# Kernel tuning notes

Hardware: AMD Instinct MI355X
Metric: run time of the kernel (lower is better)

## Reference

```python
import jax, jax.numpy as jnp
import numpy as np

H, KVH, DH = 32, 8, 128        # attention heads, kv heads, head dim (shared by both streams)
G = H // KVH                   # GQA group size
EPS = 1e-6


def rms_norm(x, w):
    xf = x.astype(jnp.float32)
    n = xf * jax.lax.rsqrt(jnp.mean(xf * xf, axis=-1, keepdims=True) + EPS)
    return (n * w).astype(x.dtype)


def apply_rope(x, positions, max_wavelength=10000.0):
    # x: [B, L, h, DH], positions: [B, L]
    d_half = x.shape[-1] // 2
    freq_exponents = (2.0 / x.shape[-1]) * jnp.arange(d_half, dtype=jnp.float32)
    timescale = max_wavelength ** freq_exponents
    radians = positions[..., None].astype(jnp.float32) / timescale          # [B, L, d_half]
    radians = radians[..., None, :]                                         # [B, L, 1, d_half]
    s, c = jnp.sin(radians), jnp.cos(radians)
    xf = x.astype(jnp.float32)
    x1, x2 = xf[..., :d_half], xf[..., d_half:]
    out = jnp.concatenate([x1 * c - x2 * s, x2 * c + x1 * s], axis=-1)
    return out.astype(x.dtype)


def setup_inputs() -> dict:
    key = jax.random.key(0)
    ks = jax.random.split(key, 16)
    B, LV, LE = 2, 1024, 64
    DV, DE = 2560, 1920
    s = 0.02
    inp = {
        "vlm_embeds": jax.random.normal(ks[0], (B, LV, DV), jnp.float32),
        "expert_embeds": jax.random.normal(ks[1], (B, LE, DE), jnp.float32),
        "position_ids": jnp.sort(jax.random.randint(ks[2], (B, LV + LE), 0, 2048), axis=-1),
        "attention_mask": jnp.ones((B, LV + LE, LV + LE), dtype=bool),
        "w_ln_vlm": jnp.ones((DV,), jnp.float32),
        "Wq_vlm": jax.random.normal(ks[3], (DV, H * DH), jnp.float32) * s,
        "Wk_vlm": jax.random.normal(ks[4], (DV, KVH * DH), jnp.float32) * s,
        "Wv_vlm": jax.random.normal(ks[5], (DV, KVH * DH), jnp.float32) * s,
        "Wo_vlm": jax.random.normal(ks[6], (H * DH, DV), jnp.float32) * s,
        "w_ln_exp": jnp.ones((DE,), jnp.float32),
        "Wq_exp": jax.random.normal(ks[7], (DE, H * DH), jnp.float32) * s,
        "Wk_exp": jax.random.normal(ks[8], (DE, KVH * DH), jnp.float32) * s,
        "Wv_exp": jax.random.normal(ks[9], (DE, KVH * DH), jnp.float32) * s,
        "Wo_exp": jax.random.normal(ks[10], (H * DH, DE), jnp.float32) * s,
    }
    return inp


def _mixed_attn_layer(vlm_embeds, expert_embeds,
                      w_ln_vlm, Wq_vlm, Wk_vlm, Wv_vlm, Wo_vlm,
                      w_ln_exp, Wq_exp, Wk_exp, Wv_exp, Wo_exp,
                      position_ids, attention_mask, knowledge_insulation=True):
    B, LV, _ = vlm_embeds.shape
    LE = expert_embeds.shape[1]

    # Stream 0: VLM prefix (knowledge insulation -> no grad into VLM path).
    hv = rms_norm(vlm_embeds, w_ln_vlm)
    qv = (hv @ Wq_vlm).reshape(B, LV, H, DH)
    kv = (hv @ Wk_vlm).reshape(B, LV, KVH, DH)
    vv = (hv @ Wv_vlm).reshape(B, LV, KVH, DH)
    if knowledge_insulation:
        qv = jax.lax.stop_gradient(qv)
        kv = jax.lax.stop_gradient(kv)
        vv = jax.lax.stop_gradient(vv)

    # Stream 1: expert suffix.
    he = rms_norm(expert_embeds, w_ln_exp)
    qe = (he @ Wq_exp).reshape(B, LE, H, DH)
    ke = (he @ Wk_exp).reshape(B, LE, KVH, DH)
    ve = (he @ Wv_exp).reshape(B, LE, KVH, DH)

    # Concatenate streams along the sequence dim, then inline RoPE on q and k.
    q = jnp.concatenate([qv, qe], axis=1)          # [B, L, 32, 128]
    k = jnp.concatenate([kv, ke], axis=1)          # [B, L, 8, 128]
    v = jnp.concatenate([vv, ve], axis=1)
    q = apply_rope(q, position_ids)
    k = apply_rope(k, position_ids)

    # Eager GQA attention in fp32 (matches _eager_attention_forward).
    k_full = jnp.repeat(k, G, axis=2)              # kv-head major, group minor
    v_full = jnp.repeat(v, G, axis=2)
    att = jnp.einsum("bqhd,bkhd->bhqk", q.astype(jnp.float32), k_full.astype(jnp.float32))
    att = att * (DH ** -0.5)
    big_neg = jnp.finfo(jnp.float32).min
    att = jnp.where(attention_mask[:, None, :, :], att, big_neg)
    probs = jax.nn.softmax(att, axis=-1).astype(v_full.dtype)
    out = jnp.einsum("bhqk,bkhd->bqhd", probs, v_full).reshape(B, LV + LE, H * DH)

    # Split back to streams, per-stream output projection + residual.
    out_vlm = vlm_embeds + out[:, :LV] @ Wo_vlm
    out_exp = expert_embeds + out[:, LV:] @ Wo_exp
    return out_vlm, out_exp


def reference(vlm_embeds, expert_embeds, position_ids, attention_mask,
              w_ln_vlm, Wq_vlm, Wk_vlm, Wv_vlm, Wo_vlm,
              w_ln_exp, Wq_exp, Wk_exp, Wv_exp, Wo_exp):
    _, out_exp = _mixed_attn_layer(
        vlm_embeds, expert_embeds,
        w_ln_vlm, Wq_vlm, Wk_vlm, Wv_vlm, Wo_vlm,
        w_ln_exp, Wq_exp, Wk_exp, Wv_exp, Wo_exp,
        position_ids, attention_mask)
    return out_exp
```

## Files before the change

### kernel.cpp

```cpp
#include <hip/hip_runtime.h>
#include <hip/hip_bf16.h>
#include <cstddef>

#define B_  2
#define LV_ 1024
#define LE_ 64
#define S_TOT 1088
#define DV_ 2560
#define DE_ 1920
#define H_  32
#define KVH_ 8
#define DH_ 128
#define HD_ 4096
#define KVD_ 1024
#define NSPL 9

typedef short short8 __attribute__((ext_vector_type(8)));
typedef float f32x4 __attribute__((ext_vector_type(4)));

typedef __hip_bfloat16 bf16;

__device__ inline float b2f(bf16 h) { return __bfloat162float(h); }
__device__ inline bf16 f2b(float f) { return __float2bfloat16(f); }

#define OFF_HVB   0ul
#define OFF_WKVT  10485760ul
#define OFF_HEB   20971520ul
#define OFF_WQKVT 21463040ul
#define OFF_QE    45056000ul
#define OFF_KBUF  46104576ul
#define OFF_VBUF  50561024ul
#define OFF_AO    59473920ul
#define OFF_P1    0ul
#define OFF_WOT   0ul
#define OFF_M     20971520ul
#define OFF_L     21118976ul
#define OFF_OP    21463040ul
#define OFF_P2    21463040ul

#define NSPLIT1 6
#define NSPLIT2 16

__global__ __launch_bounds__(256) void rmsnorm_bf16(
    const float* __restrict__ x, const float* __restrict__ w,
    bf16* __restrict__ out, int D) {
  int row = blockIdx.x;
  const float4* x4 = (const float4*)(x + (size_t)row * D);
  const float4* w4 = (const float4*)w;
  int D4 = D >> 2;
  float ss = 0.f;
  for (int i = threadIdx.x; i < D4; i += 256) {
    float4 v = x4[i];
    ss += v.x * v.x + v.y * v.y + v.z * v.z + v.w * v.w;
  }
  __shared__ float red[256];
  red[threadIdx.x] = ss; __syncthreads();
  for (int s = 128; s > 0; s >>= 1) {
    if (threadIdx.x < s) red[threadIdx.x] += red[threadIdx.x + s];
    __syncthreads();
  }
  float inv = rsqrtf(red[0] / (float)D + 1e-6f);
  ushort4* o4 = (ushort4*)(out + (size_t)row * D);
  for (int i = threadIdx.x; i < D4; i += 256) {
    float4 v = x4[i], wv = w4[i];
    bf16 a = f2b(v.x * inv * wv.x), b = f2b(v.y * inv * wv.y);
    bf16 c = f2b(v.z * inv * wv.z), d = f2b(v.w * inv * wv.w);
    ushort4 o;
    o.x = *(ushort*)&a; o.y = *(ushort*)&b; o.z = *(ushort*)&c; o.w = *(ushort*)&d;
    o4[i] = o;
  }
}

__device__ inline void tile_tconv(float (*t)[65],
    const float* __restrict__ W, bf16* __restrict__ Wt,
    int K, int N, int n_off, int bx, int by) {
  int n0 = bx * 64, k0 = by * 64;
  int tid = threadIdx.x;
  int c = tid & 63, r4 = tid >> 6;
#pragma unroll 4
  for (int it = 0; it < 16; ++it) {
    int k = it * 4 + r4;
    t[k][c] = W[(size_t)(k0 + k) * N + n0 + c];
  }
  __syncthreads();
#pragma unroll 4
  for (int it = 0; it < 16; ++it) {
    int n = it * 4 + r4;
    Wt[(size_t)(n_off + n0 + n) * K + k0 + c] = f2b(t[c][n]);
  }
}

__global__ __launch_bounds__(256) void tconv(
    const float* __restrict__ W, bf16* __restrict__ Wt,
    int K, int N, int n_off) {
  __shared__ float t[64][65];
  tile_tconv(t, W, Wt, K, N, n_off, blockIdx.x, blockIdx.y);
}

__global__ __launch_bounds__(256) void tconv_all(
    const float* __restrict__ Wk_vlm, const float* __restrict__ Wv_vlm,
    const float* __restrict__ Wq_exp, const float* __restrict__ Wk_exp,
    const float* __restrict__ Wv_exp,
    bf16* __restrict__ WkvT, bf16* __restrict__ WqkvT) {
  __shared__ float t[64][65];
  int id = blockIdx.x;
  if (id < 640)       tile_tconv(t, Wk_vlm, WkvT, DV_, KVD_, 0,    id % 16, id / 16);
  else if (id < 1280) { id -= 640;  tile_tconv(t, Wv_vlm, WkvT,  DV_, KVD_, 1024, id % 16, id / 16); }
  else if (id < 3200) { id -= 1280; tile_tconv(t, Wq_exp, WqkvT, DE_, HD_,  0,    id % 64, id / 64); }
  else if (id < 3680) { id -= 3200; tile_tconv(t, Wk_exp, WqkvT, DE_, KVD_, 4096, id % 16, id / 16); }
  else                { id -= 3680; tile_tconv(t, Wv_exp, WqkvT, DE_, KVD_, 5120, id % 16, id / 16); }
}

__global__ __launch_bounds__(256) void gemm_mfma(
    const bf16* __restrict__ A, const bf16* __restrict__ Bt,
    int M, int N, int K,
    bf16* __restrict__ p_k, bf16* __restrict__ p_v) {
  __shared__ ushort As[128][40];
  __shared__ ushort Bs[64][40];
  int tid = threadIdx.x;
  int lane = tid & 63, wid = tid >> 6;
  int wm = (wid >> 1) * 64, wn = (wid & 1) * 32;
  int m0 = blockIdx.y * 128, n0 = blockIdx.x * 64;
  int lrow = lane & 15, quad = lane >> 4;

  f32x4 acc[4][2] = {};

  int ar = tid >> 2;
  int ac = (tid & 3) * 8;
  const ushort* Aptr = (const ushort*)A + (size_t)(m0 + ar) * K + ac;
  const ushort* Bptr = (const ushort*)Bt + (size_t)(n0 + ar) * K + ac;

  for (int k0 = 0; k0 < K; k0 += 32) {
    short8 a0 = *(const short8*)(Aptr + k0);
    short8 a1 = *(const short8*)(Aptr + (size_t)64 * K + k0);
    short8 b0 = *(const short8*)(Bptr + k0);
    __syncthreads();
    *(short8*)&As[ar][ac] = a0;
    *(short8*)&As[64 + ar][ac] = a1;
    *(short8*)&Bs[ar][ac] = b0;
    __syncthreads();
    short8 af[4], bfr[2];
#pragma unroll
    for (int i = 0; i < 4; ++i)
      af[i]  = *(const short8*)&As[wm + i * 16 + lrow][quad * 8];
#pragma unroll
    for (int j = 0; j < 2; ++j)
      bfr[j] = *(const short8*)&Bs[wn + j * 16 + lrow][quad * 8];
#pragma unroll
    for (int i = 0; i < 4; ++i)
#pragma unroll
      for (int j = 0; j < 2; ++j)
        acc[i][j] = __builtin_amdgcn_mfma_f32_16x16x32_bf16(af[i], bfr[j], acc[i][j], 0, 0, 0);
  }

#pragma unroll
  for (int i = 0; i < 4; ++i) {
    int gm_base = m0 + wm + i * 16 + quad * 4;
#pragma unroll
    for (int j = 0; j < 2; ++j) {
      int gn = n0 + wn + j * 16 + lrow;
#pragma unroll
      for (int r = 0; r < 4; ++r) {
        int m = gm_base + r;
        float v = acc[i][j][r];
        int b = m >> 10, s = m & 1023;
        size_t row = (size_t)(b * S_TOT + s);
        if (gn < 1024) p_k[row * KVD_ + gn] = f2b(v);
        else           p_v[row * KVD_ + (gn - 1024)] = f2b(v);
      }
    }
  }
}

__global__ __launch_bounds__(256) void gemm_splitk(
    const bf16* __restrict__ A, const bf16* __restrict__ Bt,
    int N, int K_full, int Kc, float* __restrict__ partial) {
  __shared__ ushort As[128][40];
  __shared__ ushort Bs[64][40];
  int tid = threadIdx.x;
  int lane = tid & 63, wid = tid >> 6;
  int wm = (wid >> 1) * 64, wn = (wid & 1) * 32;
  int n0 = blockIdx.x * 64;
  int k_beg = blockIdx.y * Kc, k_end = k_beg + Kc;
  int lrow = lane & 15, quad = lane >> 4;

  f32x4 acc[4][2] = {};

  int ar = tid >> 2;
  int ac = (tid & 3) * 8;
  const ushort* Aptr = (const ushort*)A + (size_t)ar * K_full + ac;
  const ushort* Bptr = (const ushort*)Bt + (size_t)(n0 + ar) * K_full + ac;

  for (int k0 = k_beg; k0 < k_end; k0 += 32) {
    short8 a0 = *(const short8*)(Aptr + k0);
    short8 a1 = *(const short8*)(Aptr + (size_t)64 * K_full + k0);
    short8 b0 = *(const short8*)(Bptr + k0);
    __syncthreads();
    *(short8*)&As[ar][ac] = a0;
    *(short8*)&As[64 + ar][ac] = a1;
    *(short8*)&Bs[ar][ac] = b0;
    __syncthreads();
    short8 af[4], bfr[2];
#pragma unroll
    for (int i = 0; i < 4; ++i)
      af[i]  = *(const short8*)&As[wm + i * 16 + lrow][quad * 8];
#pragma unroll
    for (int j = 0; j < 2; ++j)
      bfr[j] = *(const short8*)&Bs[wn + j * 16 + lrow][quad * 8];
#pragma unroll
    for (int i = 0; i < 4; ++i)
#pragma unroll
      for (int j = 0; j < 2; ++j)
        acc[i][j] = __builtin_amdgcn_mfma_f32_16x16x32_bf16(af[i], bfr[j], acc[i][j], 0, 0, 0);
  }

  float* pbase = partial + (size_t)blockIdx.y * 128 * N;
#pragma unroll
  for (int i = 0; i < 4; ++i) {
    int m_base = wm + i * 16 + quad * 4;
#pragma unroll
    for (int j = 0; j < 2; ++j) {
      int gn = n0 + wn + j * 16 + lrow;
#pragma unroll
      for (int r = 0; r < 4; ++r)
        pbase[(size_t)(m_base + r) * N + gn] = acc[i][j][r];
    }
  }
}

__global__ __launch_bounds__(256) void reduce_qkv(
    const float* __restrict__ partial, bf16* __restrict__ qe,
    bf16* __restrict__ kbuf, bf16* __restrict__ vbuf) {
  int idx = (blockIdx.x * 256 + threadIdx.x) * 4;
  int m = idx / 6144, n = idx % 6144;
  f32x4 s = {};
#pragma unroll
  for (int sp = 0; sp < NSPLIT1; ++sp) {
    const f32x4 v = *(const f32x4*)(partial + (size_t)sp * 128 * 6144 + idx);
    s += v;
  }
  ushort4 o;
  bf16 h0 = f2b(s[0]), h1 = f2b(s[1]), h2 = f2b(s[2]), h3 = f2b(s[3]);
  o.x = *(ushort*)&h0; o.y = *(ushort*)&h1; o.z = *(ushort*)&h2; o.w = *(ushort*)&h3;
  int b = m >> 6, l = m & 63;
  if (n < 4096) {
    *(ushort4*)((ushort*)qe + (size_t)m * HD_ + n) = o;
  } else {
    size_t row = (size_t)(b * S_TOT + LV_ + l);
    if (n < 5120) *(ushort4*)((ushort*)kbuf + row * KVD_ + (n - 4096)) = o;
    else          *(ushort4*)((ushort*)vbuf + row * KVD_ + (n - 5120)) = o;
  }
}

__global__ __launch_bounds__(256) void reduce_out(
    const float* __restrict__ partial, const float* __restrict__ residual,
    float* __restrict__ out) {
  int idx = (blockIdx.x * 256 + threadIdx.x) * 4;
  f32x4 s = *(const f32x4*)(residual + idx);
#pragma unroll
  for (int sp = 0; sp < NSPLIT2; ++sp) {
    const f32x4 v = *(const f32x4*)(partial + (size_t)sp * 128 * 1920 + idx);
    s += v;
  }
  *(f32x4*)(out + idx) = s;
}

__global__ __launch_bounds__(256) void rope_fused(
    bf16* __restrict__ qe, bf16* __restrict__ kbuf,
    const int* __restrict__ pos_ids) {
  if (blockIdx.x < 128) {
    int row = blockIdx.x;
    int b = row >> 6, l = row & 63;
    float pos = (float)pos_ids[b * S_TOT + LV_ + l];
    bf16* qrow = qe + (size_t)row * HD_;
    for (int p = threadIdx.x; p < H_ * 64; p += 256) {
      int hh = p >> 6, i = p & 63;
      float inv_ts = expf(-9.210340371976184f * (float)i * (1.0f / 64.0f));
      float r = pos * inv_ts;
      float sn = sinf(r), cs = cosf(r);
      float x1 = b2f(qrow[hh * DH_ + i]), x2 = b2f(qrow[hh * DH_ + i + 64]);
      qrow[hh * DH_ + i]      = f2b(x1 * cs - x2 * sn);
      qrow[hh * DH_ + i + 64] = f2b(x2 * cs + x1 * sn);
    }
  } else {
    int bid = blockIdx.x - 128;
    int s = bid % S_TOT, b = bid / S_TOT;
    float pos = (float)pos_ids[b * S_TOT + s];
    size_t base = ((size_t)(b * S_TOT + s)) * KVD_;
    for (int t = threadIdx.x; t < KVH_ * 64; t += 256) {
      int kvh = t >> 6, i = t & 63;
      size_t idx = base + kvh * DH_ + i;
      float inv_ts = expf(-9.210340371976184f * (float)i * (1.0f / 64.0f));
      float r = pos * inv_ts;
      float sn = sinf(r), cs = cosf(r);
      float x1 = b2f(kbuf[idx]), x2 = b2f(kbuf[idx + 64]);
      kbuf[idx]      = f2b(x1 * cs - x2 * sn);
      kbuf[idx + 64] = f2b(x2 * cs + x1 * sn);
    }
  }
}

__global__ __launch_bounds__(256) void attn_part(
    const bf16* __restrict__ qe, const bf16* __restrict__ kbuf,
    const bf16* __restrict__ vbuf,
    float* __restrict__ O_p, float* __restrict__ m_arr,
    float* __restrict__ l_arr) {
  int bh = blockIdx.x & 63;
  int split = blockIdx.x >> 6;
  int h = bh & 31, b = bh >> 5;
  int kvh = h >> 2;
  int tid = threadIdx.x;
  int lane = tid & 63, wid = tid >> 6;
  int lr = lane & 15, quad = lane >> 4;

  __shared__ ushort Ks[64][152];
  __shared__ ushort vTs[128][72];
  __shared__ ushort sc[4][16][72];

  short8 qf[4];
  {
    const ushort* qptr = (const ushort*)qe +
        ((size_t)(b * LE_ + wid * 16 + lr)) * HD_ + h * DH_ + quad * 8;
#pragma unroll
    for (int ks = 0; ks < 4; ++ks) qf[ks] = *(const short8*)(qptr + ks * 32);
  }

  f32x4 Of[8] = {};
  float m_i[4], l_i[4];
#pragma unroll
  for (int r = 0; r < 4; ++r) { m_i[r] = -1e30f; l_i[r] = 0.f; }

  const float scale = 0.08838834764831845f;
  int nch = (split == 8) ? 1 : 2;

  for (int c = 0; c < nch; ++c) {
    int key0 = split * 128 + c * 64;
    __syncthreads();
    {
      int dg = tid & 15, kq = tid >> 4;
#pragma unroll
      for (int it = 0; it < 4; ++it) {
        int key = it * 16 + kq;
        short8 v = *(const short8*)((const ushort*)kbuf +
            ((size_t)(b * S_TOT + key0 + key) * KVH_ + kvh) * DH_ + dg * 8);
        *(short8*)&Ks[key][dg * 8] = v;
      }
    }
    {
      int key = tid & 63, dgrp = tid >> 6;
      const ushort* vp = (const ushort*)vbuf +
          ((size_t)(b * S_TOT + key0 + key) * KVH_ + kvh) * DH_ + dgrp * 32;
      short8 vv[4];
#pragma unroll
      for (int q8 = 0; q8 < 4; ++q8) vv[q8] = *(const short8*)(vp + q8 * 8);
#pragma unroll
      for (int q8 = 0; q8 < 4; ++q8)
#pragma unroll
        for (int j = 0; j < 8; ++j)
          vTs[dgrp * 32 + q8 * 8 + j][key] = (ushort)vv[q8][j];
    }
    __syncthreads();

    f32x4 Sf[4] = {};
#pragma unroll
    for (int kt = 0; kt < 4; ++kt)
#pragma unroll
      for (int ks = 0; ks < 4; ++ks) {
        short8 kf = *(const short8*)&Ks[kt * 16 + lr][quad * 8 + ks * 32];
        Sf[kt] = __builtin_amdgcn_mfma_f32_16x16x32_bf16(qf[ks], kf, Sf[kt], 0, 0, 0);
      }

#pragma unroll
    for (int kt = 0; kt < 4; ++kt) Sf[kt] *= scale;
#pragma unroll
    for (int r = 0; r < 4; ++r) {
      float mx = fmaxf(fmaxf(Sf[0][r], Sf[1][r]), fmaxf(Sf[2][r], Sf[3][r]));
#pragma unroll
      for (int msk = 1; msk < 16; msk <<= 1) mx = fmaxf(mx, __shfl_xor(mx, msk));
      float mn = fmaxf(m_i[r], mx);
      float alpha = __expf(m_i[r] - mn);
      m_i[r] = mn;
      float ls = 0.f;
#pragma unroll
      for (int kt = 0; kt < 4; ++kt) {
        float p = __expf(Sf[kt][r] - mn);
        Sf[kt][r] = p;
        ls += p;
      }
      l_i[r] = l_i[r] * alpha + ls;
#pragma unroll
      for (int nt = 0; nt < 8; ++nt) Of[nt][r] *= alpha;
#pragma unroll
      for (int kt = 0; kt < 4; ++kt) {
        bf16 t = f2b(Sf[kt][r]);
        sc[wid][quad * 4 + r][kt * 16 + lr] = *(ushort*)&t;
      }
    }

#pragma unroll
    for (int ks = 0; ks < 2; ++ks) {
      short8 pf = *(const short8*)&sc[wid][lr][quad * 8 + ks * 32];
#pragma unroll
      for (int nt = 0; nt < 8; ++nt) {
        short8 vf = *(const short8*)&vTs[nt * 16 + lr][quad * 8 + ks * 32];
        Of[nt] = __builtin_amdgcn_mfma_f32_16x16x32_bf16(pf, vf, Of[nt], 0, 0, 0);
      }
    }
  }

  float l_row[4];
#pragma unroll
  for (int r = 0; r < 4; ++r) {
    float l = l_i[r];
#pragma unroll
    for (int msk = 1; msk < 16; msk <<= 1) l += __shfl_xor(l, msk);
    l_row[r] = l;
  }

  size_t rbase = (size_t)split * 4096 + (size_t)bh * 64;
#pragma unroll
  for (int nt = 0; nt < 8; ++nt)
#pragma unroll
    for (int r = 0; r < 4; ++r) {
      int q = wid * 16 + quad * 4 + r;
      O_p[(rbase + q) * 128 + nt * 16 + lr] = Of[nt][r];
    }
  if (lr == 0) {
#pragma unroll
    for (int r = 0; r < 4; ++r) {
      int q = wid * 16 + quad * 4 + r;
      m_arr[rbase + q] = m_i[r];
      l_arr[rbase + q] = l_row[r];
    }
  }
}

__global__ __launch_bounds__(256) void attn_combine(
    const float* __restrict__ O_p, const float* __restrict__ m_arr,
    const float* __restrict__ l_arr, bf16* __restrict__ ao) {
  int t = blockIdx.x * 256 + threadIdx.x;
  int d = t & 127, row = t >> 7;
  float m_g = -1e30f;
#pragma unroll
  for (int s = 0; s < NSPL; ++s) m_g = fmaxf(m_g, m_arr[s * 4096 + row]);
  float denom = 0.f, acc = 0.f;
#pragma unroll
  for (int s = 0; s < NSPL; ++s) {
    float w = __expf(m_arr[s * 4096 + row] - m_g);
    denom += w * l_arr[s * 4096 + row];
    acc   += w * O_p[((size_t)s * 4096 + row) * 128 + d];
  }
  int b = row >> 11, h = (row >> 6) & 31, q = row & 63;
  bf16 o = f2b(acc / denom);
  ((ushort*)ao)[((size_t)(b * 64 + q) * 32 + h) * 128 + d] = *(ushort*)&o;
}

extern "C" void kernel_launch(void* const* d_in, const int* in_sizes, int n_in,
                              void* d_out, int out_size, void* d_ws, size_t ws_size,
                              hipStream_t stream) {
  const float* vlm      = (const float*)d_in[0];
  const float* expe     = (const float*)d_in[1];
  const int*   pos      = (const int*)d_in[2];
  const float* w_ln_vlm = (const float*)d_in[4];
  const float* Wk_vlm   = (const float*)d_in[6];
  const float* Wv_vlm   = (const float*)d_in[7];
  const float* w_ln_exp = (const float*)d_in[9];
  const float* Wq_exp   = (const float*)d_in[10];
  const float* Wk_exp   = (const float*)d_in[11];
  const float* Wv_exp   = (const float*)d_in[12];
  const float* Wo_exp   = (const float*)d_in[13];
  float* out = (float*)d_out;
  char* ws = (char*)d_ws;

  bf16* hv_b  = (bf16*)(ws + OFF_HVB);
  bf16* WkvT  = (bf16*)(ws + OFF_WKVT);
  bf16* he_b  = (bf16*)(ws + OFF_HEB);
  bf16* WqkvT = (bf16*)(ws + OFF_WQKVT);
  bf16* qe    = (bf16*)(ws + OFF_QE);
  bf16* kbuf  = (bf16*)(ws + OFF_KBUF);
  bf16* vbuf  = (bf16*)(ws + OFF_VBUF);
  bf16* ao    = (bf16*)(ws + OFF_AO);
  float* part1 = (float*)(ws + OFF_P1);
  bf16* WoT   = (bf16*)(ws + OFF_WOT);
  float* m_arr = (float*)(ws + OFF_M);
  float* l_arr = (float*)(ws + OFF_L);
  float* O_p   = (float*)(ws + OFF_OP);
  float* part2 = (float*)(ws + OFF_P2);

  rmsnorm_bf16<<<B_ * LV_, 256, 0, stream>>>(vlm, w_ln_vlm, hv_b, DV_);
  rmsnorm_bf16<<<B_ * LE_, 256, 0, stream>>>(expe, w_ln_exp, he_b, DE_);

  tconv_all<<<4160, 256, 0, stream>>>(Wk_vlm, Wv_vlm, Wq_exp, Wk_exp, Wv_exp,
                                      WkvT, WqkvT);

  gemm_mfma<<<dim3(32, 16), 256, 0, stream>>>(hv_b, WkvT, 2048, 2048, DV_,
                                              kbuf, vbuf);

  gemm_splitk<<<dim3(96, NSPLIT1), 256, 0, stream>>>(he_b, WqkvT, 6144, DE_,
                                                     DE_ / NSPLIT1, part1);
  reduce_qkv<<<128 * 6144 / 4 / 256, 256, 0, stream>>>(part1, qe, kbuf, vbuf);

  rope_fused<<<128 + B_ * S_TOT, 256, 0, stream>>>(qe, kbuf, pos);

  tconv<<<dim3(30, 64), 256, 0, stream>>>(Wo_exp, WoT, HD_, DE_, 0);

  attn_part<<<64 * NSPL, 256, 0, stream>>>(qe, kbuf, vbuf, O_p, m_arr, l_arr);
  attn_combine<<<4096 * 128 / 256, 256, 0, stream>>>(O_p, m_arr, l_arr, ao);

  gemm_splitk<<<dim3(30, NSPLIT2), 256, 0, stream>>>(ao, WoT, 1920, HD_,
                                                     HD_ / NSPLIT2, part2);
  reduce_out<<<128 * 1920 / 4 / 256, 256, 0, stream>>>(part2, expe, out);
}
```

Before: 330.3 us.

## Fuse VLM KV and expert QKV GEMMs into one pipelined LDS-DMA kernel

```diff
diff --git a/kernel.cpp b/kernel.cpp
--- a/kernel.cpp
+++ b/kernel.cpp
@@ -23,6 +23,12 @@
 __device__ inline float b2f(bf16 h) { return __bfloat162float(h); }
 __device__ inline bf16 f2b(float f) { return __float2bfloat16(f); }
 
+typedef const __attribute__((address_space(1))) void* gptr_t;
+typedef __attribute__((address_space(3))) void* lptr_t;
+__device__ inline void gl16(const void* g, void* l) {
+  __builtin_amdgcn_global_load_lds((gptr_t)g, (lptr_t)l, 16, 0, 0);
+}
+
 #define OFF_HVB   0ul
 #define OFF_WKVT  10485760ul
 #define OFF_HEB   20971520ul
@@ -31,14 +37,12 @@
 #define OFF_KBUF  46104576ul
 #define OFF_VBUF  50561024ul
 #define OFF_AO    59473920ul
-#define OFF_P1    0ul
 #define OFF_WOT   0ul
 #define OFF_M     20971520ul
 #define OFF_L     21118976ul
 #define OFF_OP    21463040ul
 #define OFF_P2    21463040ul
 
-#define NSPLIT1 6
 #define NSPLIT2 16
 
 __global__ __launch_bounds__(256) void rmsnorm_bf16(
@@ -111,62 +115,107 @@
   else                { id -= 3680; tile_tconv(t, Wv_exp, WqkvT, DE_, KVD_, 5120, id % 16, id / 16); }
 }
 
-__global__ __launch_bounds__(256) void gemm_mfma(
-    const bf16* __restrict__ A, const bf16* __restrict__ Bt,
-    int M, int N, int K,
-    bf16* __restrict__ p_k, bf16* __restrict__ p_v) {
-  __shared__ ushort As[128][40];
-  __shared__ ushort Bs[64][40];
+__global__ __launch_bounds__(256) void gemm_fused(
+    const bf16* __restrict__ hv, const bf16* __restrict__ WkvT,
+    const bf16* __restrict__ he, const bf16* __restrict__ WqkvT,
+    bf16* __restrict__ kbuf, bf16* __restrict__ vbuf, bf16* __restrict__ qe) {
+  __shared__ ushort As[3][128][32];
+  __shared__ ushort Bs[3][128][32];
   int tid = threadIdx.x;
-  int lane = tid & 63, wid = tid >> 6;
-  int wm = (wid >> 1) * 64, wn = (wid & 1) * 32;
-  int m0 = blockIdx.y * 128, n0 = blockIdx.x * 64;
-  int lrow = lane & 15, quad = lane >> 4;
-
-  f32x4 acc[4][2] = {};
-
-  int ar = tid >> 2;
-  int ac = (tid & 3) * 8;
-  const ushort* Aptr = (const ushort*)A + (size_t)(m0 + ar) * K + ac;
-  const ushort* Bptr = (const ushort*)Bt + (size_t)(n0 + ar) * K + ac;
-
-  for (int k0 = 0; k0 < K; k0 += 32) {
-    short8 a0 = *(const short8*)(Aptr + k0);
-    short8 a1 = *(const short8*)(Aptr + (size_t)64 * K + k0);
-    short8 b0 = *(const short8*)(Bptr + k0);
-    __syncthreads();
-    *(short8*)&As[ar][ac] = a0;
-    *(short8*)&As[64 + ar][ac] = a1;
-    *(short8*)&Bs[ar][ac] = b0;
-    __syncthreads();
-    short8 af[4], bfr[2];
+  int lane = tid & 63, w = tid >> 6;
+  int lr = lane & 15, quad = lane >> 4;
+  int wm = (w >> 1) * 64, wn = (w & 1) * 64;
+
+  bool expert = (blockIdx.x >= 256);
+  const ushort* Ab; const ushort* Bb; int K, nsteps, m0, n0;
+  if (!expert) {
+    m0 = (blockIdx.x >> 4) * 128; n0 = (blockIdx.x & 15) * 128;
+    Ab = (const ushort*)hv; Bb = (const ushort*)WkvT;
+    K = DV_; nsteps = DV_ / 32;
+  } else {
+    m0 = 0; n0 = (int)(blockIdx.x - 256) * 128;
+    Ab = (const ushort*)he; Bb = (const ushort*)WqkvT;
+    K = DE_; nsteps = DE_ / 32;
+  }
+
+  int r0 = w * 32 + (lane >> 2);
+  int r1 = r0 + 16;
+  int s0 = (lane & 3) ^ ((r0 >> 1) & 3);
+  int s1 = (lane & 3) ^ ((r1 >> 1) & 3);
+  const ushort* sa0 = Ab + (size_t)(m0 + r0) * K + s0 * 8;
+  const ushort* sa1 = Ab + (size_t)(m0 + r1) * K + s1 * 8;
+  const ushort* sb0 = Bb + (size_t)(n0 + r0) * K + s0 * 8;
+  const ushort* sb1 = Bb + (size_t)(n0 + r1) * K + s1 * 8;
+
+  auto STAGE = [&](int buf, int t) {
+    int k0 = t * 32;
+    gl16(sa0 + k0, &As[buf][w * 32][0]);
+    gl16(sb0 + k0, &Bs[buf][w * 32][0]);
+    gl16(sa1 + k0, &As[buf][w * 32 + 16][0]);
+    gl16(sb1 + k0, &Bs[buf][w * 32 + 16][0]);
+  };
+
+  int sslot = (quad ^ ((lr >> 1) & 3)) * 8;
+
+  f32x4 acc[4][4] = {};
+
+  STAGE(0, 0);
+  STAGE(1, 1);
+  int cur = 0, nxt = 2;
+  for (int t = 0; t < nsteps; ++t) {
+    if (t + 2 < nsteps) {
+      STAGE(nxt, t + 2);
+      asm volatile("s_waitcnt vmcnt(8)" ::: "memory");
+    } else if (t + 2 == nsteps) {
+      asm volatile("s_waitcnt vmcnt(4)" ::: "memory");
+    } else {
+      asm volatile("s_waitcnt vmcnt(0)" ::: "memory");
+    }
+    __builtin_amdgcn_s_barrier();
+
+    short8 af[4], bv[4];
+#pragma unroll
+    for (int i = 0; i < 4; ++i) {
+      af[i] = *(const short8*)&As[cur][wm + i * 16 + lr][sslot];
+      bv[i] = *(const short8*)&Bs[cur][wn + i * 16 + lr][sslot];
+    }
 #pragma unroll
     for (int i = 0; i < 4; ++i)
-      af[i]  = *(const short8*)&As[wm + i * 16 + lrow][quad * 8];
-#pragma unroll
-    for (int j = 0; j < 2; ++j)
-      bfr[j] = *(const short8*)&Bs[wn + j * 16 + lrow][quad * 8];
-#pragma unroll
-    for (int i = 0; i < 4; ++i)
-#pragma unroll
-      for (int j = 0; j < 2; ++j)
-        acc[i][j] = __builtin_amdgcn_mfma_f32_16x16x32_bf16(af[i], bfr[j], acc[i][j], 0, 0, 0);
+#pragma unroll
+      for (int j = 0; j < 4; ++j)
+        acc[i][j] = __builtin_amdgcn_mfma_f32_16x16x32_bf16(af[i], bv[j], acc[i][j], 0, 0, 0);
+
+    __builtin_amdgcn_s_barrier();
+    cur = (cur == 2) ? 0 : cur + 1;
+    nxt = (nxt == 2) ? 0 : nxt + 1;
   }
 
 #pragma unroll
   for (int i = 0; i < 4; ++i) {
-    int gm_base = m0 + wm + i * 16 + quad * 4;
-#pragma unroll
-    for (int j = 0; j < 2; ++j) {
-      int gn = n0 + wn + j * 16 + lrow;
+    int mm_base = wm + i * 16 + quad * 4;
+#pragma unroll
+    for (int j = 0; j < 4; ++j) {
+      int gn = n0 + wn + j * 16 + lr;
 #pragma unroll
       for (int r = 0; r < 4; ++r) {
-        int m = gm_base + r;
+        int mm = mm_base + r;
         float v = acc[i][j][r];
-        int b = m >> 10, s = m & 1023;
-        size_t row = (size_t)(b * S_TOT + s);
-        if (gn < 1024) p_k[row * KVD_ + gn] = f2b(v);
-        else           p_v[row * KVD_ + (gn - 1024)] = f2b(v);
+        if (!expert) {
+          int m = m0 + mm;
+          int b = m >> 10, s = m & 1023;
+          size_t row = (size_t)(b * S_TOT + s);
+          if (gn < 1024) kbuf[row * KVD_ + gn] = f2b(v);
+          else           vbuf[row * KVD_ + (gn - 1024)] = f2b(v);
+        } else {
+          int b = mm >> 6, l = mm & 63;
+          if (gn < 4096) {
+            qe[(size_t)mm * HD_ + gn] = f2b(v);
+          } else {
+            size_t row = (size_t)(b * S_TOT + LV_ + l);
+            if (gn < 5120) kbuf[row * KVD_ + (gn - 4096)] = f2b(v);
+            else           vbuf[row * KVD_ + (gn - 5120)] = f2b(v);
+          }
+        }
       }
     }
   }
@@ -225,30 +274,6 @@
       for (int r = 0; r < 4; ++r)
         pbase[(size_t)(m_base + r) * N + gn] = acc[i][j][r];
     }
-  }
-}
-
-__global__ __launch_bounds__(256) void reduce_qkv(
-    const float* __restrict__ partial, bf16* __restrict__ qe,
-    bf16* __restrict__ kbuf, bf16* __restrict__ vbuf) {
-  int idx = (blockIdx.x * 256 + threadIdx.x) * 4;
-  int m = idx / 6144, n = idx % 6144;
-  f32x4 s = {};
-#pragma unroll
-  for (int sp = 0; sp < NSPLIT1; ++sp) {
-    const f32x4 v = *(const f32x4*)(partial + (size_t)sp * 128 * 6144 + idx);
-    s += v;
-  }
-  ushort4 o;
-  bf16 h0 = f2b(s[0]), h1 = f2b(s[1]), h2 = f2b(s[2]), h3 = f2b(s[3]);
-  o.x = *(ushort*)&h0; o.y = *(ushort*)&h1; o.z = *(ushort*)&h2; o.w = *(ushort*)&h3;
-  int b = m >> 6, l = m & 63;
-  if (n < 4096) {
-    *(ushort4*)((ushort*)qe + (size_t)m * HD_ + n) = o;
-  } else {
-    size_t row = (size_t)(b * S_TOT + LV_ + l);
-    if (n < 5120) *(ushort4*)((ushort*)kbuf + row * KVD_ + (n - 4096)) = o;
-    else          *(ushort4*)((ushort*)vbuf + row * KVD_ + (n - 5120)) = o;
   }
 }
 
@@ -480,7 +505,6 @@
   bf16* kbuf  = (bf16*)(ws + OFF_KBUF);
   bf16* vbuf  = (bf16*)(ws + OFF_VBUF);
   bf16* ao    = (bf16*)(ws + OFF_AO);
-  float* part1 = (float*)(ws + OFF_P1);
   bf16* WoT   = (bf16*)(ws + OFF_WOT);
   float* m_arr = (float*)(ws + OFF_M);
   float* l_arr = (float*)(ws + OFF_L);
@@ -493,12 +517,7 @@
   tconv_all<<<4160, 256, 0, stream>>>(Wk_vlm, Wv_vlm, Wq_exp, Wk_exp, Wv_exp,
                                       WkvT, WqkvT);
 
-  gemm_mfma<<<dim3(32, 16), 256, 0, stream>>>(hv_b, WkvT, 2048, 2048, DV_,
-                                              kbuf, vbuf);
-
-  gemm_splitk<<<dim3(96, NSPLIT1), 256, 0, stream>>>(he_b, WqkvT, 6144, DE_,
-                                                     DE_ / NSPLIT1, part1);
-  reduce_qkv<<<128 * 6144 / 4 / 256, 256, 0, stream>>>(part1, qe, kbuf, vbuf);
+  gemm_fused<<<304, 256, 0, stream>>>(hv_b, WkvT, he_b, WqkvT, kbuf, vbuf, qe);
 
   rope_fused<<<128 + B_ * S_TOT, 256, 0, stream>>>(qe, kbuf, pos);
 
```

Result: faster. 317.8 us (-3.8%).
